# Kernel tuning notes

Measured on AMD Instinct MI355X. Metric: run time of the kernel, lower is better.

## Reference

```python
import math
import jax, jax.numpy as jnp
import numpy as np

Q = 24
N = 8
T_THETA = 1.0
R_S = 3.0
SIGMA_R = 1.0
RHO_MIN = 0.05
N_ORI = 4
TOL = 0.5


def _build_bank_7x7(n, tol=0.5, eps=1e-06):
    m = 3
    coords = np.arange(-m, m + 1, dtype=np.float32)
    u = coords.reshape(1, 1, 7)  # varies along width
    v = coords.reshape(1, 7, 1)  # varies along height
    Delta = math.pi / float(n)
    thetas = ((0.5 * Delta + np.arange(n, dtype=np.float32) * Delta) % math.pi).reshape(n, 1, 1)
    d = np.abs(-np.sin(thetas) * u + np.cos(thetas) * v)
    M = (d <= tol).astype(np.float32)
    M[:, m, m] = 1.0
    W = M[:, None, :, :]  # (n,1,7,7)
    denom = W.sum(axis=(1, 2, 3), keepdims=True) + eps
    return W / denom


def _bilinear_shift(Fm, dx, dy):
    """Shift-sample Fm (B,H,W) by (dx,dy) pixels, matching torch grid_sample
    (bilinear, zeros padding, align_corners=False) on linspace(-1,1) base grid."""
    B, H, W = Fm.shape
    xs = (jnp.arange(W, dtype=Fm.dtype) - dx) * (W / (W - 1)) - 0.5
    ys = (jnp.arange(H, dtype=Fm.dtype) - dy) * (H / (H - 1)) - 0.5

    def axis_parts(p, size):
        p0 = jnp.floor(p)
        f = p - p0
        i0 = p0.astype(jnp.int32)
        i1 = i0 + 1
        w0 = jnp.where((i0 >= 0) & (i0 < size), 1.0 - f, 0.0)
        w1 = jnp.where((i1 >= 0) & (i1 < size), f, 0.0)
        return jnp.clip(i0, 0, size - 1), jnp.clip(i1, 0, size - 1), w0, w1

    y0, y1, wy0, wy1 = axis_parts(ys, H)
    x0, x1, wx0, wx1 = axis_parts(xs, W)
    # separable bilinear: interpolate rows, then columns
    Fy = Fm[:, y0, :] * wy0[None, :, None] + Fm[:, y1, :] * wy1[None, :, None]
    return Fy[:, :, x0] * wx0[None, None, :] + Fy[:, :, x1] * wx1[None, None, :]


def _line_energy_theta(x):
    """x: (B,2,H,W) -> hat_theta (B,H,W) in [0, 2pi)."""
    Fm = jnp.sqrt(jnp.sum(x * x, axis=1))  # (B,H,W) L2 over channels
    t_n = jnp.arange(1, N + 1, dtype=x.dtype) / N * R_S
    w_n = jnp.exp(-t_n * t_n / (2.0 * SIGMA_R ** 2))
    w_n = w_n / w_n.sum()
    theta_q = 2.0 * jnp.pi * jnp.arange(Q, dtype=x.dtype) / Q
    cos_q, sin_q = jnp.cos(theta_q), jnp.sin(theta_q)

    def energy_one_angle(cs):
        c, s = cs
        # (N,B,H,W) samples along the ray, then radial weighted sum
        S = jax.vmap(lambda t: _bilinear_shift(Fm, t * c, t * s))(t_n)
        return jnp.tensordot(w_n, S, axes=1)  # (B,H,W)

    E = jax.lax.map(energy_one_angle, (cos_q, sin_q))  # (Q,B,H,W)
    pi_q = jax.nn.softmax(E / T_THETA, axis=0)
    sy = jnp.einsum('q,qbhw->bhw', sin_q, pi_q)
    cx = jnp.einsum('q,qbhw->bhw', cos_q, pi_q)
    hat = jnp.arctan2(sy, cx)
    return jnp.remainder(hat + 2.0 * jnp.pi, 2.0 * jnp.pi)


def setup_inputs() -> dict:
    key = jax.random.key(0)
    k1, = jax.random.split(key, 1)
    x = jax.random.normal(k1, (8, 2, 512, 512), dtype=jnp.float32)
    gain = jnp.ones((1,), dtype=jnp.float32)
    log_route_temp = jnp.asarray(math.log(0.08), dtype=jnp.float32)
    rho_scaled = (0.5 - RHO_MIN) / (1.0 - RHO_MIN)
    rho_logit = jnp.asarray(math.log(rho_scaled / (1.0 - rho_scaled)), dtype=jnp.float32)
    W_bank = jnp.asarray(_build_bank_7x7(N_ORI, tol=TOL))  # (4,1,7,7)
    Delta = math.pi / float(N_ORI)
    centers = (0.5 * Delta + np.arange(N_ORI, dtype=np.float32) * Delta).reshape(1, N_ORI, 1, 1)
    theta_centers = jnp.asarray(centers)
    return {"x": x, "gain": gain, "log_route_temp": log_route_temp,
            "rho_logit": rho_logit, "W_bank": W_bank, "theta_centers": theta_centers}


def reference(x, gain, log_route_temp, rho_logit, W_bank, theta_centers):
    hat_theta = _line_energy_theta(x)  # (B,H,W)
    # orientation bank conv: expand (n,1,7,7) -> (n,2,7,7), SAME padding (pad=3)
    w = jnp.broadcast_to(W_bank, (N_ORI, 2, 7, 7))
    y = jax.lax.conv_general_dilated(
        x, w, window_strides=(1, 1), padding=((3, 3), (3, 3)),
        dimension_numbers=('NCHW', 'OIHW', 'NCHW'))  # (B,n,H,W)
    # soft orientation routing
    theta = jnp.remainder(hat_theta, jnp.pi)[:, None, :, :]  # (B,1,H,W)
    delta = jnp.remainder(theta - theta_centers + 0.5 * jnp.pi, jnp.pi) - 0.5 * jnp.pi
    dist = jnp.abs(delta)  # (B,n,H,W)
    route_temp = jnp.clip(jnp.exp(log_route_temp), 0.001, 2.0)
    base = jax.nn.softmax(-dist / route_temp, axis=1)
    rho = jax.nn.sigmoid(rho_logit) * (1.0 - RHO_MIN) + RHO_MIN
    gamma = 1.0 / (rho + 1e-08)
    sharp = jnp.power(base + 1e-12, gamma)
    weights = sharp / (sharp.sum(axis=1, keepdims=True) + 1e-08)
    out = jnp.sum(y * weights, axis=1, keepdims=True)  # (B,1,H,W)
    return jnp.clip(gain, 0.001, None) * out
```

## Files before the change

kernel.cpp:

```cpp
#include <hip/hip_runtime.h>
#include <math.h>

#define HALO 4
#define TWX 72
#define TWY 12
#define NST (TWX*TWY)

#if __has_builtin(__builtin_amdgcn_fractf)
#define FRACTF(x) __builtin_amdgcn_fractf(x)
#else
#define FRACTF(x) ((x) - floorf(x))
#endif
#if __has_builtin(__builtin_amdgcn_exp2f)
#define EXP2F(x) __builtin_amdgcn_exp2f(x)
#else
#define EXP2F(x) exp2f(x)
#endif
#if __has_builtin(__builtin_amdgcn_logf)
#define LOG2F(x) __builtin_amdgcn_logf(x)
#else
#define LOG2F(x) log2f(x)
#endif

__global__ __launch_bounds__(64) void gp_setup(const float* __restrict__ gain,
                                               const float* __restrict__ lrt,
                                               const float* __restrict__ rlg,
                                               const float* __restrict__ Wb,
                                               float* __restrict__ tbl) {
  int t = threadIdx.x;
  __shared__ float wtmp[8];
  if (t < 8) {
    float tn = (float)(t + 1) * 0.375f;
    wtmp[t] = expf(-0.5f * tn * tn);
  }
  if (t < 24) {
    float th = (6.283185307179586f * (float)t) / 24.0f;
    float c = cosf(th), s = sinf(th);
    const float sc = (float)(512.0 / 511.0);
    tbl[t] = c; tbl[24 + t] = s; tbl[48 + t] = c * sc; tbl[72 + t] = s * sc;
  }
  __syncthreads();
  if (t == 0) {
    const float L2E = 1.44269504088896340736f;
    float sum = 0.f;
    for (int n = 0; n < 8; ++n) sum += wtmp[n];
    for (int n = 0; n < 8; ++n) tbl[96 + n] = (wtmp[n] / sum) * L2E;
    float rt = expf(lrt[0]);
    rt = fminf(fmaxf(rt, 0.001f), 2.0f);
    float sg = 1.0f / (1.0f + expf(-rlg[0]));
    float rho = sg * 0.95f + 0.05f;
    tbl[104] = (1.0f / rt) * L2E;
    tbl[105] = 1.0f / (rho + 1e-8f);
    tbl[106] = fmaxf(gain[0], 0.001f);

    const int K0[7] = {14,15,23,24,25,33,34};
    const int K1[7] = {2,9,17,24,31,39,46};
    const int K2[7] = {4,11,17,24,31,37,44};
    const int K3[7] = {19,20,23,24,25,28,29};
    const int* KK[4] = {K0,K1,K2,K3};
    int ok = 1;
    for (int o = 0; o < 4; ++o) {
      float w0v = Wb[o * 49 + KK[o][0]];
      if (w0v == 0.f) ok = 0;
      unsigned long long mask = 0;
      for (int t2 = 0; t2 < 7; ++t2) mask |= 1ull << KK[o][t2];
      for (int k = 0; k < 49; ++k) {
        float w = Wb[o * 49 + k];
        int nz = (w != 0.f);
        int want = (int)((mask >> k) & 1ull);
        if (nz != want) ok = 0;
        if (nz && w != w0v) ok = 0;
      }
      tbl[180 + o] = w0v;
    }
    ((int*)tbl)[172] = ok;
  }
}

__device__ inline float finish(float SY, float CX, float a0, float a1, float a2,
                               float a3, const float* __restrict__ cen,
                               float irt2, float gamma, float gainc) {
  const float TP  = 6.283185307179586f;
  const float PIF = 3.14159265358979323846f;
  const float HP  = 1.57079632679489661923f;
  float hat = atan2f(SY, CX);
  float r1 = hat + TP;
  r1 = (r1 >= TP) ? (r1 - TP) : r1;
  float theta = (r1 >= PIF) ? (r1 - PIF) : r1;
  float dist[4];
  #pragma unroll
  for (int o = 0; o < 4; ++o) {
    float d = theta - cen[o] + HP;
    d -= (d >= PIF) ? PIF : 0.f;
    d += (d < 0.f) ? PIF : 0.f;
    dist[o] = fabsf(d - HP);
  }
  float mn = fminf(fminf(dist[0], dist[1]), fminf(dist[2], dist[3]));
  float m2 = mn * irt2;
  float eo[4], Z = 0.f;
  #pragma unroll
  for (int o = 0; o < 4; ++o) { eo[o] = EXP2F(fmaf(-irt2, dist[o], m2)); Z += eo[o]; }
  float invZ = 1.0f / Z;
  float sh[4], Zs = 0.f;
  #pragma unroll
  for (int o = 0; o < 4; ++o) {
    sh[o] = EXP2F(gamma * LOG2F(fmaf(eo[o], invZ, 1e-12f)));
    Zs += sh[o];
  }
  float wsi = 1.0f / (Zs + 1e-8f);
  return gainc * ((a0 * sh[0] + a1 * sh[1] + a2 * sh[2] + a3 * sh[3]) * wsi);
}

__global__ __launch_bounds__(256) void gp_main7(const float* __restrict__ x,
                                                const float* __restrict__ Wb,
                                                const float* __restrict__ cen,
                                                const float* __restrict__ tbl,
                                                float* __restrict__ out) {
  __shared__ float  Fm[NST];
  __shared__ float  Sm[NST];
  __shared__ float4 Qd[NST];

  const int tx = threadIdx.x;
  const int ty = threadIdx.y;
  const int tid = ty * 64 + tx;
  const int bx0 = blockIdx.x * 64 - HALO;
  const int by0 = blockIdx.y * 4 - HALO;
  const int b = blockIdx.z;
  const float* __restrict__ x0p = x + (size_t)b * 2 * 512 * 512;
  const float* __restrict__ x1p = x0p + 512 * 512;

  #pragma unroll
  for (int it = 0; it < 4; ++it) {
    int idx = tid + it * 256;
    if (idx < NST) {
      int r = idx / TWX, c = idx - r * TWX;
      int gy = by0 + r, gx = bx0 + c;
      float a = 0.f, bv = 0.f;
      if ((unsigned)gx < 512u && (unsigned)gy < 512u) {
        size_t o = (size_t)gy * 512 + gx;
        a = x0p[o]; bv = x1p[o];
      }
      Fm[idx] = sqrtf(a * a + bv * bv);
      Sm[idx] = a + bv;
    }
  }
  __syncthreads();
  #pragma unroll
  for (int it = 0; it < 4; ++it) {
    int idx = tid + it * 256;
    if (idx < NST) {
      int r = idx / TWX, c = idx - r * TWX;
      int r1 = (r < TWY - 1) ? r + 1 : r;
      int c1 = (c < TWX - 1) ? c + 1 : c;
      float v00 = Fm[r * TWX + c],  v01 = Fm[r * TWX + c1];
      float v10 = Fm[r1 * TWX + c], v11 = Fm[r1 * TWX + c1];
      Qd[idx] = make_float4(v00, v01 - v00, v10 - v00, (v11 - v10) - (v01 - v00));
    }
  }
  __syncthreads();

  const int gi = bx0 + HALO + tx;
  const int gj = by0 + HALO + ty;
  const float SC = (float)(512.0 / 511.0);
  const float axl = fmaf((float)gi, SC, -0.5f) - (float)bx0;
  const float ayl = fmaf((float)gj, SC, -0.5f) - (float)by0;

  float wn[8];
  #pragma unroll
  for (int n = 0; n < 8; ++n) wn[n] = tbl[96 + n];

  float SY = 0.f, CX = 0.f;
  for (int q = 0; q < 24; ++q) {
    const float cs = tbl[48 + q];
    const float sn = tbl[72 + q];
    float e2 = 0.f;
    int offp = -1;
    float4 v = make_float4(0.f, 0.f, 0.f, 0.f);
    #pragma unroll
    for (int n = 0; n < 8; ++n) {
      const float tn = 0.375f * (float)(n + 1);
      float px = fmaf(-cs, tn, axl);
      float py = fmaf(-sn, tn, ayl);
      int ix = (int)px, iy = (int)py;
      float fx = FRACTF(px), fy = FRACTF(py);
      int off = iy * TWX + ix;
      if (off != offp) {
        v = Qd[off];
        offp = off;
      }
      float s = fmaf(fy, fmaf(fx, v.w, v.z), fmaf(fx, v.y, v.x));
      e2 = fmaf(wn[n], s, e2);
    }
    float e = EXP2F(e2);
    SY = fmaf(e, tbl[24 + q], SY);
    CX = fmaf(e, tbl[q], CX);
  }

  const int* ti = (const int*)tbl;
  const int ccen = (ty + 4) * TWX + tx + 4;
  float a0, a1, a2, a3;
  if (ti[172]) {
    float sCt = Sm[ccen];
    float H3 = (Sm[ccen - 1] + sCt) + Sm[ccen + 1];
    float V3 = (Sm[ccen - TWX] + sCt) + Sm[ccen + TWX];
    a0 = tbl[180] * (H3 + ((Sm[ccen - 75] + Sm[ccen - 74]) + (Sm[ccen + 74] + Sm[ccen + 75])));
    a1 = tbl[181] * (V3 + ((Sm[ccen - 217] + Sm[ccen - 145]) + (Sm[ccen + 145] + Sm[ccen + 217])));
    a2 = tbl[182] * (V3 + ((Sm[ccen - 215] + Sm[ccen - 143]) + (Sm[ccen + 143] + Sm[ccen + 215])));
    a3 = tbl[183] * (H3 + ((Sm[ccen - 70] + Sm[ccen - 69]) + (Sm[ccen + 69] + Sm[ccen + 70])));
  } else {
    a0 = a1 = a2 = a3 = 0.f;
    for (int kj = 0; kj < 7; ++kj)
      for (int ki = 0; ki < 7; ++ki) {
        float s = Sm[(ty + 1 + kj) * TWX + (tx + 1 + ki)];
        int k = kj * 7 + ki;
        a0 = fmaf(s, Wb[k], a0); a1 = fmaf(s, Wb[49 + k], a1);
        a2 = fmaf(s, Wb[98 + k], a2); a3 = fmaf(s, Wb[147 + k], a3);
      }
  }

  const float irt2  = tbl[104];
  const float gamma = tbl[105];
  const float gainc = tbl[106];
  float ov = finish(SY, CX, a0, a1, a2, a3, cen, irt2, gamma, gainc);
  out[((size_t)b * 512 + gj) * 512 + gi] = ov;
}

extern "C" void kernel_launch(void* const* d_in, const int* in_sizes, int n_in,
                              void* d_out, int out_size, void* d_ws, size_t ws_size,
                              hipStream_t stream) {
  const float* x    = (const float*)d_in[0];
  const float* gain = (const float*)d_in[1];
  const float* lrt  = (const float*)d_in[2];
  const float* rlg  = (const float*)d_in[3];
  const float* Wb   = (const float*)d_in[4];
  const float* cen  = (const float*)d_in[5];
  float* tbl = (float*)d_ws;

  gp_setup<<<1, 64, 0, stream>>>(gain, lrt, rlg, Wb, tbl);

  dim3 grid(8, 128, 8);
  dim3 blk(64, 4);
  gp_main7<<<grid, blk, 0, stream>>>(x, Wb, cen, tbl, (float*)d_out);
}
```

Baseline: 153.8 us.

## Precompute global bilinear quad image and split ray samples between LDS and global

Adds a pre-pass kernel that writes a padded global image of bilinear quad coefficients (value plus x, y and cross differences) for every pixel. The main kernel copies its tile of this image into LDS instead of computing it there. The three outermost ray samples now read straight from the global quad image (via cache) while the five inner ones read LDS, which spreads load between the two paths. Workgroup indices are swizzled to improve cache locality. This adds an extra kernel launch and roughly 70 MB of workspace traffic, with a fallback kernel used when the workspace is too small.

Measured after the change: 151.7 us. About the same (-1.3%).

```diff
diff --git a/kernel.cpp b/kernel.cpp
--- a/kernel.cpp
+++ b/kernel.cpp
@@ -5,6 +5,10 @@
 #define TWX 72
 #define TWY 12
 #define NST (TWX*TWY)
+#define QIW 528
+#define QIH 520
+
+typedef float f4 __attribute__((ext_vector_type(4)));
 
 #if __has_builtin(__builtin_amdgcn_fractf)
 #define FRACTF(x) __builtin_amdgcn_fractf(x)
@@ -77,6 +81,60 @@
   }
 }
 
+__device__ inline float fmv(const float* __restrict__ x0p, const float* __restrict__ x1p,
+                            int Y, int X) {
+  int cY = min(max(Y, 0), 511);
+  int cX = min(max(X, 0), 511);
+  size_t o = (size_t)cY * 512 + cX;
+  float a = x0p[o], b = x1p[o];
+  float f = sqrtf(a * a + b * b);
+  return ((unsigned)X < 512u && (unsigned)Y < 512u) ? f : 0.f;
+}
+
+__global__ __launch_bounds__(256) void gp_quadF(const float* __restrict__ x,
+                                                f4* __restrict__ qimg) {
+  int g = blockIdx.x * 256 + threadIdx.x;
+  if (g >= QIH * 132) return;
+  int b = blockIdx.y;
+  int y = g / 132, xg = g - y * 132;
+  int X = xg * 4 - 4, Y = y - 4;
+  const float* __restrict__ x0p = x + (size_t)b * 2 * 512 * 512;
+  const float* __restrict__ x1p = x0p + 512 * 512;
+
+  float F0[5], F1[5];
+  if (X >= 0 && X <= 507 && Y >= 0 && Y <= 510) {
+    size_t r0 = (size_t)Y * 512 + X, r1 = r0 + 512;
+    f4 a0 = *(const f4*)(x0p + r0); float a4 = x0p[r0 + 4];
+    f4 b0 = *(const f4*)(x1p + r0); float b4 = x1p[r0 + 4];
+    f4 c0 = *(const f4*)(x0p + r1); float c4 = x0p[r1 + 4];
+    f4 d0 = *(const f4*)(x1p + r1); float d4 = x1p[r1 + 4];
+    #pragma unroll
+    for (int i = 0; i < 4; ++i) {
+      F0[i] = sqrtf(a0[i] * a0[i] + b0[i] * b0[i]);
+      F1[i] = sqrtf(c0[i] * c0[i] + d0[i] * d0[i]);
+    }
+    F0[4] = sqrtf(a4 * a4 + b4 * b4);
+    F1[4] = sqrtf(c4 * c4 + d4 * d4);
+  } else {
+    #pragma unroll
+    for (int i = 0; i < 5; ++i) {
+      F0[i] = fmv(x0p, x1p, Y, X + i);
+      F1[i] = fmv(x0p, x1p, Y + 1, X + i);
+    }
+  }
+  f4* dst = qimg + (size_t)(b * QIH + y) * QIW + xg * 4;
+  #pragma unroll
+  for (int k = 0; k < 4; ++k) {
+    float d0 = F0[k + 1] - F0[k];
+    f4 q;
+    q[0] = F0[k];
+    q[1] = d0;
+    q[2] = F1[k] - F0[k];
+    q[3] = (F1[k + 1] - F1[k]) - d0;
+    dst[k] = q;
+  }
+}
+
 __device__ inline float finish(float SY, float CX, float a0, float a1, float a2,
                                float a3, const float* __restrict__ cen,
                                float irt2, float gamma, float gainc) {
@@ -111,24 +169,58 @@
   return gainc * ((a0 * sh[0] + a1 * sh[1] + a2 * sh[2] + a3 * sh[3]) * wsi);
 }
 
-__global__ __launch_bounds__(256) void gp_main7(const float* __restrict__ x,
+#define TN0 0.375f
+#define TN1 0.75f
+#define TN2 1.125f
+#define TN3 1.5f
+#define TN4 1.875f
+#define TN5 2.25f
+#define TN6 2.625f
+#define TN7 3.0f
+
+#define CRD(n) \
+  float px##n = fmaf(-cs, TN##n, axl); \
+  float py##n = fmaf(-sn, TN##n, ayl); \
+  int   ix##n = (int)px##n; \
+  int   iy##n = (int)py##n; \
+  float fx##n = FRACTF(px##n); \
+  float fy##n = FRACTF(py##n);
+
+#define BILERP(v, n) fmaf(fy##n, fmaf(fx##n, v.w, v.z), fmaf(fx##n, v.y, v.x))
+#define BILERP4(v, n) fmaf(fy##n, fmaf(fx##n, v[3], v[2]), fmaf(fx##n, v[1], v[0]))
+
+__global__ __launch_bounds__(256) void gp_main8(const float* __restrict__ x,
+                                                const f4* __restrict__ qimg,
                                                 const float* __restrict__ Wb,
                                                 const float* __restrict__ cen,
                                                 const float* __restrict__ tbl,
                                                 float* __restrict__ out) {
-  __shared__ float  Fm[NST];
-  __shared__ float  Sm[NST];
-  __shared__ float4 Qd[NST];
+  __shared__ f4    Qd[NST];
+  __shared__ float Sm[NST];
 
   const int tx = threadIdx.x;
   const int ty = threadIdx.y;
   const int tid = ty * 64 + tx;
-  const int bx0 = blockIdx.x * 64 - HALO;
-  const int by0 = blockIdx.y * 4 - HALO;
-  const int b = blockIdx.z;
+  int wg = blockIdx.x;
+  int swz = (wg & 7) * 1024 + (wg >> 3);
+  int bx = swz & 7;
+  int by = (swz >> 3) & 127;
+  int b  = swz >> 10;
+
+  const int bx0 = bx * 64 - HALO;
+  const int by0 = by * 4 - HALO;
   const float* __restrict__ x0p = x + (size_t)b * 2 * 512 * 512;
   const float* __restrict__ x1p = x0p + 512 * 512;
-
+  const f4* __restrict__ qg = qimg + (size_t)(b * QIH + by * 4) * QIW + bx * 64;
+
+  #pragma unroll
+  for (int it = 0; it < 4; ++it) {
+    int idx = tid + it * 256;
+    if (idx < NST) {
+      int r = idx / TWX, c = idx - r * TWX;
+      Qd[idx] = qg[r * QIW + c];
+    }
+  }
   #pragma unroll
   for (int it = 0; it < 4; ++it) {
     int idx = tid + it * 256;
@@ -140,21 +232,7 @@
         size_t o = (size_t)gy * 512 + gx;
         a = x0p[o]; bv = x1p[o];
       }
-      Fm[idx] = sqrtf(a * a + bv * bv);
       Sm[idx] = a + bv;
-    }
-  }
-  __syncthreads();
-  #pragma unroll
-  for (int it = 0; it < 4; ++it) {
-    int idx = tid + it * 256;
-    if (idx < NST) {
-      int r = idx / TWX, c = idx - r * TWX;
-      int r1 = (r < TWY - 1) ? r + 1 : r;
-      int c1 = (c < TWX - 1) ? c + 1 : c;
-      float v00 = Fm[r * TWX + c],  v01 = Fm[r * TWX + c1];
-      float v10 = Fm[r1 * TWX + c], v11 = Fm[r1 * TWX + c1];
-      Qd[idx] = make_float4(v00, v01 - v00, v10 - v00, (v11 - v10) - (v01 - v00));
     }
   }
   __syncthreads();
@@ -165,32 +243,33 @@
   const float axl = fmaf((float)gi, SC, -0.5f) - (float)bx0;
   const float ayl = fmaf((float)gj, SC, -0.5f) - (float)by0;
 
-  float wn[8];
-  #pragma unroll
-  for (int n = 0; n < 8; ++n) wn[n] = tbl[96 + n];
+  const float wn0 = tbl[96], wn1 = tbl[97], wn2 = tbl[98], wn3 = tbl[99];
+  const float wn4 = tbl[100], wn5 = tbl[101], wn6 = tbl[102], wn7 = tbl[103];
 
   float SY = 0.f, CX = 0.f;
   for (int q = 0; q < 24; ++q) {
     const float cs = tbl[48 + q];
     const float sn = tbl[72 + q];
-    float e2 = 0.f;
-    int offp = -1;
-    float4 v = make_float4(0.f, 0.f, 0.f, 0.f);
-    #pragma unroll
-    for (int n = 0; n < 8; ++n) {
-      const float tn = 0.375f * (float)(n + 1);
-      float px = fmaf(-cs, tn, axl);
-      float py = fmaf(-sn, tn, ayl);
-      int ix = (int)px, iy = (int)py;
-      float fx = FRACTF(px), fy = FRACTF(py);
-      int off = iy * TWX + ix;
-      if (off != offp) {
-        v = Qd[off];
-        offp = off;
-      }
-      float s = fmaf(fy, fmaf(fx, v.w, v.z), fmaf(fx, v.y, v.x));
-      e2 = fmaf(wn[n], s, e2);
-    }
+    CRD(5) CRD(6) CRD(7)
+    f4 B5 = qg[iy5 * QIW + ix5];
+    f4 B6 = qg[iy6 * QIW + ix6];
+    f4 B7 = qg[iy7 * QIW + ix7];
+    CRD(0) CRD(1) CRD(2) CRD(3) CRD(4)
+    f4 A0 = Qd[iy0 * TWX + ix0];
+    f4 A1 = Qd[iy1 * TWX + ix1];
+    f4 A2 = Qd[iy2 * TWX + ix2];
+    f4 A3 = Qd[iy3 * TWX + ix3];
+    f4 A4 = Qd[iy4 * TWX + ix4];
+    float e2 = wn0 * BILERP4(A0, 0);
+    e2 = fmaf(wn1, BILERP4(A1, 1), e2);
+    e2 = fmaf(wn2, BILERP4(A2, 2), e2);
+    e2 = fmaf(wn3, BILERP4(A3, 3), e2);
+    e2 = fmaf(wn4, BILERP4(A4, 4), e2);
+    asm volatile("" : : "v"(B5), "v"(B6), "v"(B7));
+    e2 = fmaf(wn5, BILERP4(B5, 5), e2);
+    e2 = fmaf(wn6, BILERP4(B6, 6), e2);
+    e2 = fmaf(wn7, BILERP4(B7, 7), e2);
+
     float e = EXP2F(e2);
     SY = fmaf(e, tbl[24 + q], SY);
     CX = fmaf(e, tbl[q], CX);
@@ -225,6 +304,109 @@
   out[((size_t)b * 512 + gj) * 512 + gi] = ov;
 }
 
+__global__ __launch_bounds__(256) void gp_main_fb(const float* __restrict__ x,
+                                                  const float* __restrict__ Wb,
+                                                  const float* __restrict__ cen,
+                                                  const float* __restrict__ tbl,
+                                                  float* __restrict__ out) {
+  __shared__ float Fm[NST];
+  __shared__ float Sm[NST];
+  __shared__ f4    Qd[NST];
+  const int tx = threadIdx.x;
+  const int ty = threadIdx.y;
+  const int tid = ty * 64 + tx;
+  const int bx0 = blockIdx.x * 64 - HALO;
+  const int by0 = blockIdx.y * 4 - HALO;
+  const int b = blockIdx.z;
+  const float* __restrict__ x0p = x + (size_t)b * 2 * 512 * 512;
+  const float* __restrict__ x1p = x0p + 512 * 512;
+  #pragma unroll
+  for (int it = 0; it < 4; ++it) {
+    int idx = tid + it * 256;
+    if (idx < NST) {
+      int r = idx / TWX, c = idx - r * TWX;
+      int gy = by0 + r, gx = bx0 + c;
+      float a = 0.f, bv = 0.f;
+      if ((unsigned)gx < 512u && (unsigned)gy < 512u) {
+        size_t o = (size_t)gy * 512 + gx;
+        a = x0p[o]; bv = x1p[o];
+      }
+      Fm[idx] = sqrtf(a * a + bv * bv);
+      Sm[idx] = a + bv;
+    }
+  }
+  __syncthreads();
+  #pragma unroll
+  for (int it = 0; it < 4; ++it) {
+    int idx = tid + it * 256;
+    if (idx < NST) {
+      int r = idx / TWX, c = idx - r * TWX;
+      int r1 = (r < TWY - 1) ? r + 1 : r;
+      int c1 = (c < TWX - 1) ? c + 1 : c;
+      float v00 = Fm[r * TWX + c],  v01 = Fm[r * TWX + c1];
+      float v10 = Fm[r1 * TWX + c], v11 = Fm[r1 * TWX + c1];
+      f4 qv; qv[0] = v00; qv[1] = v01 - v00; qv[2] = v10 - v00;
+      qv[3] = (v11 - v10) - (v01 - v00);
+      Qd[idx] = qv;
+    }
+  }
+  __syncthreads();
+  const int gi = bx0 + HALO + tx;
+  const int gj = by0 + HALO + ty;
+  const float SC = (float)(512.0 / 511.0);
+  const float axl = fmaf((float)gi, SC, -0.5f) - (float)bx0;
+  const float ayl = fmaf((float)gj, SC, -0.5f) - (float)by0;
+  float wn[8];
+  #pragma unroll
+  for (int n = 0; n < 8; ++n) wn[n] = tbl[96 + n];
+  float SY = 0.f, CX = 0.f;
+  for (int q = 0; q < 24; ++q) {
+    const float csx = tbl[48 + q];
+    const float ssy = tbl[72 + q];
+    float e2 = 0.f;
+    #pragma unroll
+    for (int n = 0; n < 8; ++n) {
+      const float tn = 0.375f * (float)(n + 1);
+      float px = fmaf(-csx, tn, axl);
+      float py = fmaf(-ssy, tn, ayl);
+      int ix = (int)px, iy = (int)py;
+      float fx = FRACTF(px), fy = FRACTF(py);
+      f4 v = Qd[iy * TWX + ix];
+      float s = fmaf(fy, fmaf(fx, v[3], v[2]), fmaf(fx, v[1], v[0]));
+      e2 = fmaf(wn[n], s, e2);
+    }
+    float e = EXP2F(e2);
+    SY = fmaf(e, tbl[24 + q], SY);
+    CX = fmaf(e, tbl[q], CX);
+  }
+  const int* ti = (const int*)tbl;
+  const int ccen = (ty + 4) * TWX + tx + 4;
+  float a0, a1, a2, a3;
+  if (ti[172]) {
+    float sCt = Sm[ccen];
+    float H3 = (Sm[ccen - 1] + sCt) + Sm[ccen + 1];
+    float V3 = (Sm[ccen - TWX] + sCt) + Sm[ccen + TWX];
+    a0 = tbl[180] * (H3 + ((Sm[ccen - 75] + Sm[ccen - 74]) + (Sm[ccen + 74] + Sm[ccen + 75])));
+    a1 = tbl[181] * (V3 + ((Sm[ccen - 217] + Sm[ccen - 145]) + (Sm[ccen + 145] + Sm[ccen + 217])));
+    a2 = tbl[182] * (V3 + ((Sm[ccen - 215] + Sm[ccen - 143]) + (Sm[ccen + 143] + Sm[ccen + 215])));
+    a3 = tbl[183] * (H3 + ((Sm[ccen - 70] + Sm[ccen - 69]) + (Sm[ccen + 69] + Sm[ccen + 70])));
+  } else {
+    a0 = a1 = a2 = a3 = 0.f;
+    for (int kj = 0; kj < 7; ++kj)
+      for (int ki = 0; ki < 7; ++ki) {
+        float s = Sm[(ty + 1 + kj) * TWX + (tx + 1 + ki)];
+        int k = kj * 7 + ki;
+        a0 = fmaf(s, Wb[k], a0); a1 = fmaf(s, Wb[49 + k], a1);
+        a2 = fmaf(s, Wb[98 + k], a2); a3 = fmaf(s, Wb[147 + k], a3);
+      }
+  }
+  const float irt2  = tbl[104];
+  const float gamma = tbl[105];
+  const float gainc = tbl[106];
+  float ov = finish(SY, CX, a0, a1, a2, a3, cen, irt2, gamma, gainc);
+  out[((size_t)b * 512 + gj) * 512 + gi] = ov;
+}
+
 extern "C" void kernel_launch(void* const* d_in, const int* in_sizes, int n_in,
                               void* d_out, int out_size, void* d_ws, size_t ws_size,
                               hipStream_t stream) {
@@ -238,7 +420,12 @@
 
   gp_setup<<<1, 64, 0, stream>>>(gain, lrt, rlg, Wb, tbl);
 
-  dim3 grid(8, 128, 8);
-  dim3 blk(64, 4);
-  gp_main7<<<grid, blk, 0, stream>>>(x, Wb, cen, tbl, (float*)d_out);
-}
+  size_t need = 4096 + (size_t)8 * QIH * QIW * sizeof(f4);
+  if (ws_size >= need) {
+    f4* qimg = (f4*)((char*)d_ws + 4096);
+    gp_quadF<<<dim3((QIH * 132 + 255) / 256, 8), 256, 0, stream>>>(x, qimg);
+    gp_main8<<<dim3(8192), dim3(64, 4), 0, stream>>>(x, qimg, Wb, cen, tbl, (float*)d_out);
+  } else {
+    gp_main_fb<<<dim3(8, 128, 8), dim3(64, 4), 0, stream>>>(x, Wb, cen, tbl, (float*)d_out);
+  }
+}
```
